# Optimization experiments

Hardware: AMD Instinct MI355X
Metric: run time of the kernel (lower is better)

Reference implementation:

```python
import jax, jax.numpy as jnp
import numpy as np

N, E = 50000, 800000
F_IN, HID, OUT, H = 128, 32, 4, 8
NEG_SLOPE = 0.2


def gat_conv(x, src, dst, W, a_src, a_dst, b):
    """PyG GATConv (concat=True, eval mode). x: [N,Fin]; src/dst: [E'] (self-loops included).
    W: [Fin, Hh*C]; a_src/a_dst: [Hh, C]; b: [Hh*C]."""
    n = x.shape[0]
    Hh, C = a_src.shape
    h = (x @ W).reshape(n, Hh, C)                      # [N,H,C]
    alpha_src = jnp.einsum('nhc,hc->nh', h, a_src)     # [N,H]
    alpha_dst = jnp.einsum('nhc,hc->nh', h, a_dst)     # [N,H]
    alpha = jax.nn.leaky_relu(alpha_src[src] + alpha_dst[dst], NEG_SLOPE)  # [E',H]
    # segment softmax over incoming edges of each dst node
    amax = jax.ops.segment_max(alpha, dst, num_segments=n)  # [N,H]
    ex = jnp.exp(alpha - amax[dst])
    denom = jax.ops.segment_sum(ex, dst, num_segments=n)    # [N,H]
    w = ex / (denom[dst] + 1e-16)                            # [E',H]
    msg = h[src] * w[:, :, None]                             # [E',H,C]
    out = jax.ops.segment_sum(msg, dst, num_segments=n)     # [N,H,C]
    return out.reshape(n, Hh * C) + b


def setup_inputs() -> dict:
    key = jax.random.key(0)
    ks = jax.random.split(key, 9)
    x = jax.random.normal(ks[0], (N, F_IN), jnp.float32)
    # random edge list without self loops (PyG GATConv removes then re-adds self loops)
    rng = np.random.default_rng(0)
    s = rng.integers(0, N, size=E)
    d = rng.integers(0, N, size=E)
    d = np.where(d == s, (d + 1) % N, d)
    edge_index = jnp.asarray(np.stack([s, d]), dtype=jnp.int32)
    g = lambda k, shape, fan: jax.random.normal(k, shape, jnp.float32) * (1.0 / np.sqrt(fan))
    W1 = g(ks[1], (F_IN, H * HID), F_IN)
    a_src1 = g(ks[2], (H, HID), HID)
    a_dst1 = g(ks[3], (H, HID), HID)
    b1 = jnp.zeros((H * HID,), jnp.float32)
    W2 = g(ks[4], (H * HID, H * OUT), H * HID)
    a_src2 = g(ks[5], (H, OUT), OUT)
    a_dst2 = g(ks[6], (H, OUT), OUT)
    b2 = jnp.zeros((H * OUT,), jnp.float32)
    return {"x": x, "edge_index": edge_index, "W1": W1, "a_src1": a_src1,
            "a_dst1": a_dst1, "b1": b1, "W2": W2, "a_src2": a_src2,
            "a_dst2": a_dst2, "b2": b2}


def reference(x, edge_index, W1, a_src1, a_dst1, b1, W2, a_src2, a_dst2, b2):
    n = x.shape[0]
    loops = jnp.arange(n, dtype=edge_index.dtype)
    src = jnp.concatenate([edge_index[0], loops])
    dst = jnp.concatenate([edge_index[1], loops])
    # layer 1 (dropout_edge / dropout are no-ops in eval mode)
    h = gat_conv(x, src, dst, W1, a_src1, a_dst1, b1)
    h = jax.nn.leaky_relu(h, NEG_SLOPE)
    # final layer (concat=True per the original code) -> [N, OUT*H]
    out = gat_conv(h, src, dst, W2, a_src2, a_dst2, b2)
    return out
```

## Files before the change

### kernel.cpp

```cpp
#include <hip/hip_runtime.h>
#include <hip/hip_bf16.h>
#include <cstdint>
#include <cstddef>


__device__ __forceinline__ float lrelu(float a) { return a > 0.f ? a : 0.2f * a; }

__device__ __forceinline__ unsigned short f2bf(float f) {
  unsigned u = __float_as_uint(f);
  unsigned r = (u + 0x7fff + ((u >> 16) & 1)) >> 16;
  return (unsigned short)r;
}
__device__ __forceinline__ float bf_lo(unsigned q) { return __uint_as_float(q << 16); }
__device__ __forceinline__ float bf_hi(unsigned q) { return __uint_as_float(q & 0xffff0000u); }

typedef __attribute__((ext_vector_type(8))) short bf16x8;
typedef __attribute__((ext_vector_type(4))) float f32x4;

#define ROWCAP 64


__global__ __launch_bounds__(256) void k_scatter(const int* __restrict__ srce,
                                                 const int* __restrict__ dste, int E, int n,
                                                 int* __restrict__ cursor,
                                                 int* __restrict__ srcs,
                                                 const float* __restrict__ W1,
                                                 unsigned short* __restrict__ W1T,
                                                 const float* __restrict__ W2,
                                                 unsigned short* __restrict__ W2T) {
  int t = blockIdx.x * 256 + threadIdx.x;
  if (t < E + n) {
    int s, d;
    if (t < E) { s = srce[t]; d = dste[t]; } else { s = d = t - E; }
    int pos = atomicAdd(&cursor[d], 1);
    srcs[(d << 6) + pos] = s;
  }
  if (t < 32768) {
    int k = t >> 8;
    int nn = t & 255;
    W1T[nn * 128 + k] = f2bf(W1[k * 256 + nn]);
  }
  if (t < 8192) {
    int k = t >> 5;
    int nn = t & 31;
    W2T[nn * 256 + k] = f2bf(W2[k * 32 + nn]);
  }
}


__global__ __launch_bounds__(256) void gemm1_mfma(const float* __restrict__ X,
                                                  const unsigned short* __restrict__ WT,
                                                  const float* __restrict__ a_src,
                                                  const float* __restrict__ a_dst,
                                                  unsigned short* __restrict__ h1,
                                                  float* __restrict__ a_s1,
                                                  float* __restrict__ a_d1,
                                                  int M) {
  __shared__ unsigned short As[64 * 136];
  __shared__ unsigned short Bs[256 * 72];
  const int row0 = blockIdx.x * 64;
  const int tid = threadIdx.x;
  const int wv = tid >> 6, lane = tid & 63;
  const int quad = lane >> 4, l15 = lane & 15;
  const int colw = wv * 64;

#pragma unroll
  for (int i = 0; i < 8; i++) {
    int j = tid + 256 * i;
    int r = j >> 5;
    int c4 = (j & 31) * 4;
    float4 v = make_float4(0.f, 0.f, 0.f, 0.f);
    if (row0 + r < M) v = *(const float4*)&X[(size_t)(row0 + r) * 128 + c4];
    uint2 p;
    p.x = (unsigned)f2bf(v.x) | ((unsigned)f2bf(v.y) << 16);
    p.y = (unsigned)f2bf(v.z) | ((unsigned)f2bf(v.w) << 16);
    *(uint2*)&As[r * 136 + c4] = p;
  }

  f32x4 acc[16];
#pragma unroll
  for (int i = 0; i < 16; i++) acc[i] = (f32x4)0.f;

  for (int kc = 0; kc < 128; kc += 64) {
    __syncthreads();
#pragma unroll
    for (int i = 0; i < 8; i++) {
      int j = tid + 256 * i;
      int nn = j >> 3;
      int kg = (j & 7) * 8;
      *(uint4*)&Bs[nn * 72 + kg] = *(const uint4*)&WT[nn * 128 + kc + kg];
    }
    __syncthreads();
#pragma unroll
    for (int ks = 0; ks < 64; ks += 32) {
      bf16x8 af[4], bfr[4];
#pragma unroll
      for (int mi = 0; mi < 4; mi++)
        af[mi] = *(const bf16x8*)&As[(mi * 16 + l15) * 136 + kc + ks + quad * 8];
#pragma unroll
      for (int ni = 0; ni < 4; ni++)
        bfr[ni] = *(const bf16x8*)&Bs[(colw + ni * 16 + l15) * 72 + ks + quad * 8];
#pragma unroll
      for (int mi = 0; mi < 4; mi++)
#pragma unroll
        for (int ni = 0; ni < 4; ni++)
          acc[mi * 4 + ni] = __builtin_amdgcn_mfma_f32_16x16x32_bf16(
              af[mi], bfr[ni], acc[mi * 4 + ni], 0, 0, 0);
    }
  }

  float as_[4], ad_[4];
#pragma unroll
  for (int ni = 0; ni < 4; ni++) {
    int nn = colw + ni * 16 + l15;
    as_[ni] = a_src[nn];
    ad_[ni] = a_dst[nn];
  }
  const int h0 = colw >> 5;
#pragma unroll
  for (int mi = 0; mi < 4; mi++) {
#pragma unroll
    for (int r = 0; r < 4; r++) {
      int m = row0 + mi * 16 + quad * 4 + r;
      bool valid = (m < M);
      if (valid) {
#pragma unroll
        for (int ni = 0; ni < 4; ni++)
          h1[(size_t)m * 256 + colw + ni * 16 + l15] = f2bf(acc[mi * 4 + ni][r]);
      }
      float s0 = fmaf(acc[mi * 4 + 0][r], as_[0], acc[mi * 4 + 1][r] * as_[1]);
      float s1 = fmaf(acc[mi * 4 + 2][r], as_[2], acc[mi * 4 + 3][r] * as_[3]);
      float d0 = fmaf(acc[mi * 4 + 0][r], ad_[0], acc[mi * 4 + 1][r] * ad_[1]);
      float d1 = fmaf(acc[mi * 4 + 2][r], ad_[2], acc[mi * 4 + 3][r] * ad_[3]);
#pragma unroll
      for (int mk = 1; mk <= 8; mk <<= 1) {
        s0 += __shfl_xor(s0, mk);
        s1 += __shfl_xor(s1, mk);
        d0 += __shfl_xor(d0, mk);
        d1 += __shfl_xor(d1, mk);
      }
      if (l15 == 0 && valid) {
        a_s1[m * 8 + h0]     = s0;
        a_s1[m * 8 + h0 + 1] = s1;
        a_d1[m * 8 + h0]     = d0;
        a_d1[m * 8 + h0 + 1] = d1;
      }
    }
  }
}


__global__ __launch_bounds__(256) void gemm2_mfma(const unsigned short* __restrict__ Xb,
                                                  const unsigned short* __restrict__ W2T,
                                                  const float* __restrict__ a_src,
                                                  const float* __restrict__ a_dst,
                                                  unsigned short* __restrict__ h2,
                                                  float* __restrict__ a_s2,
                                                  float* __restrict__ a_d2, int M) {
  __shared__ unsigned short As[64 * 264];
  __shared__ unsigned short Bs[32 * 264];
  const int row0 = blockIdx.x * 64;
  const int tid = threadIdx.x;
  const int wv = tid >> 6, lane = tid & 63;
  const int quad = lane >> 4, l15 = lane & 15;

#pragma unroll
  for (int i = 0; i < 8; i++) {
    int j = tid + 256 * i;
    int r = j >> 5;
    int c8 = (j & 31) * 8;
    uint4 v = make_uint4(0, 0, 0, 0);
    if (row0 + r < M) v = *(const uint4*)&Xb[(size_t)(row0 + r) * 256 + c8];
    *(uint4*)&As[r * 264 + c8] = v;
  }
#pragma unroll
  for (int i = 0; i < 4; i++) {
    int j = tid + 256 * i;
    int nn = j >> 5;
    int kg = (j & 31) * 8;
    *(uint4*)&Bs[nn * 264 + kg] = *(const uint4*)&W2T[nn * 256 + kg];
  }
  __syncthreads();

  f32x4 acc[2];
  acc[0] = (f32x4)0.f;
  acc[1] = (f32x4)0.f;
  const int mr = wv * 16;
#pragma unroll
  for (int ks = 0; ks < 256; ks += 32) {
    bf16x8 af = *(const bf16x8*)&As[(mr + l15) * 264 + ks + quad * 8];
    bf16x8 b0 = *(const bf16x8*)&Bs[(l15) * 264 + ks + quad * 8];
    bf16x8 b1 = *(const bf16x8*)&Bs[(16 + l15) * 264 + ks + quad * 8];
    acc[0] = __builtin_amdgcn_mfma_f32_16x16x32_bf16(af, b0, acc[0], 0, 0, 0);
    acc[1] = __builtin_amdgcn_mfma_f32_16x16x32_bf16(af, b1, acc[1], 0, 0, 0);
  }

  float as_[2], ad_[2];
#pragma unroll
  for (int ni = 0; ni < 2; ni++) {
    int c = ni * 16 + l15;
    as_[ni] = a_src[c];
    ad_[ni] = a_dst[c];
  }
#pragma unroll
  for (int r = 0; r < 4; r++) {
    int m = row0 + mr + quad * 4 + r;
    bool valid = (m < M);
    float s0 = acc[0][r] * as_[0];
    float s1 = acc[1][r] * as_[1];
    float d0 = acc[0][r] * ad_[0];
    float d1 = acc[1][r] * ad_[1];
#pragma unroll
    for (int mk = 1; mk <= 2; mk <<= 1) {
      s0 += __shfl_xor(s0, mk);
      s1 += __shfl_xor(s1, mk);
      d0 += __shfl_xor(d0, mk);
      d1 += __shfl_xor(d1, mk);
    }
    if (valid) {
      h2[(size_t)m * 32 + l15]      = f2bf(acc[0][r]);
      h2[(size_t)m * 32 + 16 + l15] = f2bf(acc[1][r]);
      if ((l15 & 3) == 0) {
        int hq = l15 >> 2;
        a_s2[m * 8 + hq]     = s0;
        a_s2[m * 8 + 4 + hq] = s1;
        a_d2[m * 8 + hq]     = d0;
        a_d2[m * 8 + 4 + hq] = d1;
      }
    }
  }
}


__global__ __launch_bounds__(256) void gat_agg_l1(const unsigned short* __restrict__ h,
                                                  const float* __restrict__ asrc,
                                                  const float* __restrict__ adst,
                                                  const int* __restrict__ rowcnt,
                                                  const int* __restrict__ srcs,
                                                  const float* __restrict__ bias,
                                                  unsigned short* __restrict__ out, int n) {
  int wave = threadIdx.x >> 6;
  int lane = threadIdx.x & 63;
  int d = blockIdx.x * 4 + wave;
  if (d >= n) return;
  int begin = d << 6;
  int end = begin + rowcnt[d];
  int hh = lane & 7;
  float ad = adst[d * 8 + hh];

  const int myhead = lane >> 3;
  float denom = 0.f;
  float4 acc0 = make_float4(0.f, 0.f, 0.f, 0.f);
  float4 acc1 = make_float4(0.f, 0.f, 0.f, 0.f);
#define ACCA(ff, qq)                                        \
    acc0.x = fmaf(ff, bf_lo(qq.x), acc0.x);                 \
    acc0.y = fmaf(ff, bf_hi(qq.x), acc0.y);                 \
    acc0.z = fmaf(ff, bf_lo(qq.y), acc0.z);                 \
    acc0.w = fmaf(ff, bf_hi(qq.y), acc0.w);
#define ACCB(ff, qq)                                        \
    acc1.x = fmaf(ff, bf_lo(qq.x), acc1.x);                 \
    acc1.y = fmaf(ff, bf_hi(qq.x), acc1.y);                 \
    acc1.z = fmaf(ff, bf_lo(qq.y), acc1.z);                 \
    acc1.w = fmaf(ff, bf_hi(qq.y), acc1.w);

  int e = begin;
  for (; e + 16 <= end; e += 16) {
    int s[16];
#pragma unroll
    for (int j = 0; j < 16; j++) s[j] = srcs[e + j];
    float w[16];
    if (lane < 8) {
#pragma unroll
      for (int j = 0; j < 16; j++) {
        w[j] = __expf(lrelu(asrc[s[j] * 8 + lane] + ad));
        denom += w[j];
      }
    } else {
#pragma unroll
      for (int j = 0; j < 16; j++) w[j] = 0.f;
    }
    uint2 q[16];
#pragma unroll
    for (int j = 0; j < 16; j++) q[j] = *(const uint2*)&h[(size_t)s[j] * 256 + lane * 4];
    float f[16];
#pragma unroll
    for (int j = 0; j < 16; j++) f[j] = __shfl(w[j], myhead);
#pragma unroll
    for (int j = 0; j < 16; j += 2) {
      ACCA(f[j], q[j])
      ACCB(f[j + 1], q[j + 1])
    }
  }
  for (; e < end; e += 8) {
    int s[8];
    float w[8];
#pragma unroll
    for (int j = 0; j < 8; j++) {
      int ee = e + j;
      s[j] = srcs[ee < end ? ee : end - 1];
    }
    if (lane < 8) {
#pragma unroll
      for (int j = 0; j < 8; j++) {
        float v = __expf(lrelu(asrc[s[j] * 8 + lane] + ad));
        w[j] = (e + j < end) ? v : 0.f;
        denom += w[j];
      }
    } else {
#pragma unroll
      for (int j = 0; j < 8; j++) w[j] = 0.f;
    }
    uint2 q[8];
#pragma unroll
    for (int j = 0; j < 8; j++) q[j] = *(const uint2*)&h[(size_t)s[j] * 256 + lane * 4];
    float f[8];
#pragma unroll
    for (int j = 0; j < 8; j++) f[j] = __shfl(w[j], myhead);
#pragma unroll
    for (int j = 0; j < 8; j += 2) {
      ACCA(f[j], q[j])
      ACCB(f[j + 1], q[j + 1])
    }
  }
#undef ACCA
#undef ACCB
  float4 acc;
  acc.x = acc0.x + acc1.x;
  acc.y = acc0.y + acc1.y;
  acc.z = acc0.z + acc1.z;
  acc.w = acc0.w + acc1.w;
  float dn = __shfl(denom, myhead) + 1e-16f;
  float inv = 1.f / dn;
  int f = lane * 4;
  float4 bv = *(const float4*)&bias[f];
  float rx = lrelu(acc.x * inv + bv.x);
  float ry = lrelu(acc.y * inv + bv.y);
  float rz = lrelu(acc.z * inv + bv.z);
  float rw = lrelu(acc.w * inv + bv.w);
  uint2 p;
  p.x = (unsigned)f2bf(rx) | ((unsigned)f2bf(ry) << 16);
  p.y = (unsigned)f2bf(rz) | ((unsigned)f2bf(rw) << 16);
  *(uint2*)&out[(size_t)d * 256 + f] = p;
}

__global__ __launch_bounds__(256) void gat_agg_l2(const unsigned short* __restrict__ h,
                                                  const float* __restrict__ asrc,
                                                  const float* __restrict__ adst,
                                                  const int* __restrict__ rowcnt,
                                                  const int* __restrict__ srcs,
                                                  const float* __restrict__ bias,
                                                  float* __restrict__ out, int n) {
  int wave = threadIdx.x >> 6;
  int lane = threadIdx.x & 63;
  int d = blockIdx.x * 4 + wave;
  if (d >= n) return;
  int begin = d << 6;
  int end = begin + rowcnt[d];
  int hh = lane & 7;
  int eg = lane >> 3;
  float ad = adst[d * 8 + hh];

  float denom = 0.f;
  float4 acc = make_float4(0.f, 0.f, 0.f, 0.f);
  for (int base = begin; base < end; base += 32) {
    int eA = base + eg;
    int eB = base + 8 + eg;
    int eC = base + 16 + eg;
    int eD = base + 24 + eg;
    bool vA = eA < end, vB = eB < end, vC = eC < end, vD = eD < end;
    int sA = srcs[vA ? eA : begin];
    int sB = srcs[vB ? eB : begin];
    int sC = srcs[vC ? eC : begin];
    int sD = srcs[vD ? eD : begin];
    float aA = asrc[sA * 8 + hh];
    float aB = asrc[sB * 8 + hh];
    float aC = asrc[sC * 8 + hh];
    float aD = asrc[sD * 8 + hh];
    uint2 qA = *(const uint2*)&h[(size_t)sA * 32 + hh * 4];
    uint2 qB = *(const uint2*)&h[(size_t)sB * 32 + hh * 4];
    uint2 qC = *(const uint2*)&h[(size_t)sC * 32 + hh * 4];
    uint2 qD = *(const uint2*)&h[(size_t)sD * 32 + hh * 4];
    float wA = vA ? __expf(lrelu(aA + ad)) : 0.f;
    float wB = vB ? __expf(lrelu(aB + ad)) : 0.f;
    float wC = vC ? __expf(lrelu(aC + ad)) : 0.f;
    float wD = vD ? __expf(lrelu(aD + ad)) : 0.f;
    denom += (wA + wB) + (wC + wD);
    acc.x = fmaf(wA, bf_lo(qA.x), acc.x); acc.y = fmaf(wA, bf_hi(qA.x), acc.y);
    acc.z = fmaf(wA, bf_lo(qA.y), acc.z); acc.w = fmaf(wA, bf_hi(qA.y), acc.w);
    acc.x = fmaf(wB, bf_lo(qB.x), acc.x); acc.y = fmaf(wB, bf_hi(qB.x), acc.y);
    acc.z = fmaf(wB, bf_lo(qB.y), acc.z); acc.w = fmaf(wB, bf_hi(qB.y), acc.w);
    acc.x = fmaf(wC, bf_lo(qC.x), acc.x); acc.y = fmaf(wC, bf_hi(qC.x), acc.y);
    acc.z = fmaf(wC, bf_lo(qC.y), acc.z); acc.w = fmaf(wC, bf_hi(qC.y), acc.w);
    acc.x = fmaf(wD, bf_lo(qD.x), acc.x); acc.y = fmaf(wD, bf_hi(qD.x), acc.y);
    acc.z = fmaf(wD, bf_lo(qD.y), acc.z); acc.w = fmaf(wD, bf_hi(qD.y), acc.w);
  }
#pragma unroll
  for (int mask = 8; mask <= 32; mask <<= 1) {
    denom += __shfl_xor(denom, mask);
    acc.x += __shfl_xor(acc.x, mask);
    acc.y += __shfl_xor(acc.y, mask);
    acc.z += __shfl_xor(acc.z, mask);
    acc.w += __shfl_xor(acc.w, mask);
  }
  if (lane < 8) {
    float inv = 1.f / (denom + 1e-16f);
    int f = lane * 4;
    float4 bv = *(const float4*)&bias[f];
    float4 r;
    r.x = acc.x * inv + bv.x;
    r.y = acc.y * inv + bv.y;
    r.z = acc.z * inv + bv.z;
    r.w = acc.w * inv + bv.w;
    *(float4*)&out[(size_t)d * 32 + f] = r;
  }
}


extern "C" void kernel_launch(void* const* d_in, const int* in_sizes, int n_in,
                              void* d_out, int out_size, void* d_ws, size_t ws_size,
                              hipStream_t stream) {
  const float* x   = (const float*)d_in[0];
  const int*   ei  = (const int*)d_in[1];
  const float* W1  = (const float*)d_in[2];
  const float* as1 = (const float*)d_in[3];
  const float* ad1 = (const float*)d_in[4];
  const float* b1  = (const float*)d_in[5];
  const float* W2  = (const float*)d_in[6];
  const float* as2 = (const float*)d_in[7];
  const float* ad2 = (const float*)d_in[8];
  const float* b2  = (const float*)d_in[9];
  float* out = (float*)d_out;

  const int E = in_sizes[1] / 2;
  const int n = in_sizes[0] / 128;
  const int* srce = ei;
  const int* dste = ei + E;

  char* ws = (char*)d_ws;
  size_t off = 0;
  auto alloc = [&](size_t bytes) -> void* {
    void* p = ws + off;
    off = (off + bytes + 255) & ~(size_t)255;
    return p;
  };
  int* cursor   = (int*)alloc((size_t)n * 4);
  int* srcs     = (int*)alloc((size_t)n * ROWCAP * 4);
  unsigned short* h1  = (unsigned short*)alloc((size_t)n * 256 * 2);
  unsigned short* w1t = (unsigned short*)alloc((size_t)256 * 128 * 2);
  unsigned short* w2t = (unsigned short*)alloc((size_t)32 * 256 * 2);
  float* a_s1   = (float*)alloc((size_t)n * 8 * 4);
  float* a_d1   = (float*)alloc((size_t)n * 8 * 4);
  unsigned short* x2 = (unsigned short*)alloc((size_t)n * 256 * 2);
  unsigned short* h2 = (unsigned short*)alloc((size_t)n * 32 * 2);
  float* a_s2   = (float*)alloc((size_t)n * 8 * 4);
  float* a_d2   = (float*)alloc((size_t)n * 8 * 4);

  const int tot = E + n;
  hipMemsetAsync(cursor, 0, (size_t)n * 4, stream);
  k_scatter<<<(tot + 255) / 256, 256, 0, stream>>>(srce, dste, E, n, cursor, srcs,
                                                   W1, w1t, W2, w2t);

  gemm1_mfma<<<(n + 63) / 64, 256, 0, stream>>>(x, w1t, as1, ad1, h1, a_s1, a_d1, n);
  gat_agg_l1<<<(n + 3) / 4, 256, 0, stream>>>(h1, a_s1, a_d1, cursor, srcs, b1, x2, n);

  gemm2_mfma<<<(n + 63) / 64, 256, 0, stream>>>(x2, w2t, as2, ad2, h2, a_s2, a_d2, n);
  gat_agg_l2<<<(n + 3) / 4, 256, 0, stream>>>(h2, a_s2, a_d2, cursor, srcs, b2, out, n);
}
```

Measured before the change: 268.4 us.

## Fold attention vectors into weights and compute per-lane softmax weights in aggregation

Precomputes W·a_src and W·a_dst as extra 16-column bf16 weight matrices so both GEMMs produce the attention logits with one additional MFMA, replacing the shuffle-reduction epilogues. In the layer-1 aggregation kernel, every lane now computes its own head's exp weight and denominator instead of 8 lanes computing and broadcasting via shuffles. This trades shuffles and serial dependencies for redundant exp and asrc loads (8x duplicated per head), and rounds the folded attention weights to bf16, which may reduce logit precision.

```diff
diff --git a/kernel.cpp b/kernel.cpp
--- a/kernel.cpp
+++ b/kernel.cpp
@@ -27,7 +27,13 @@
                                                  const float* __restrict__ W1,
                                                  unsigned short* __restrict__ W1T,
                                                  const float* __restrict__ W2,
-                                                 unsigned short* __restrict__ W2T) {
+                                                 unsigned short* __restrict__ W2T,
+                                                 const float* __restrict__ as1,
+                                                 const float* __restrict__ ad1,
+                                                 const float* __restrict__ as2,
+                                                 const float* __restrict__ ad2,
+                                                 unsigned short* __restrict__ Wa1T,
+                                                 unsigned short* __restrict__ Wa2T) {
   int t = blockIdx.x * 256 + threadIdx.x;
   if (t < E + n) {
     int s, d;
@@ -45,19 +51,39 @@
     int nn = t & 31;
     W2T[nn * 256 + k] = f2bf(W2[k * 32 + nn]);
   }
+  if (t < 2048) {
+    int j = t >> 7;
+    int k = t & 127;
+    const float* av = (j < 8) ? &as1[j * 32] : &ad1[(j - 8) * 32];
+    const float* wv = &W1[k * 256 + (j & 7) * 32];
+    float s = 0.f;
+#pragma unroll
+    for (int c = 0; c < 32; c++) s += wv[c] * av[c];
+    Wa1T[j * 128 + k] = f2bf(s);
+  }
+  if (t < 4096) {
+    int j = t >> 8;
+    int k = t & 255;
+    const float* av = (j < 8) ? &as2[j * 4] : &ad2[(j - 8) * 4];
+    const float* wv = &W2[k * 32 + (j & 7) * 4];
+    float s = 0.f;
+#pragma unroll
+    for (int c = 0; c < 4; c++) s += wv[c] * av[c];
+    Wa2T[j * 256 + k] = f2bf(s);
+  }
 }
 
 
 __global__ __launch_bounds__(256) void gemm1_mfma(const float* __restrict__ X,
                                                   const unsigned short* __restrict__ WT,
-                                                  const float* __restrict__ a_src,
-                                                  const float* __restrict__ a_dst,
+                                                  const unsigned short* __restrict__ WaT,
                                                   unsigned short* __restrict__ h1,
                                                   float* __restrict__ a_s1,
                                                   float* __restrict__ a_d1,
                                                   int M) {
   __shared__ unsigned short As[64 * 136];
   __shared__ unsigned short Bs[256 * 72];
+  __shared__ unsigned short Was[16 * 72];
   const int row0 = blockIdx.x * 64;
   const int tid = threadIdx.x;
   const int wv = tid >> 6, lane = tid & 63;
@@ -80,6 +106,7 @@
   f32x4 acc[16];
 #pragma unroll
   for (int i = 0; i < 16; i++) acc[i] = (f32x4)0.f;
+  f32x4 acca = (f32x4)0.f;
 
   for (int kc = 0; kc < 128; kc += 64) {
     __syncthreads();
@@ -90,6 +117,11 @@
       int kg = (j & 7) * 8;
       *(uint4*)&Bs[nn * 72 + kg] = *(const uint4*)&WT[nn * 128 + kc + kg];
     }
+    if (tid < 128) {
+      int j = tid >> 3;
+      int kg = (tid & 7) * 8;
+      *(uint4*)&Was[j * 72 + kg] = *(const uint4*)&WaT[j * 128 + kc + kg];
+    }
     __syncthreads();
 #pragma unroll
     for (int ks = 0; ks < 64; ks += 32) {
@@ -106,45 +138,30 @@
         for (int ni = 0; ni < 4; ni++)
           acc[mi * 4 + ni] = __builtin_amdgcn_mfma_f32_16x16x32_bf16(
               af[mi], bfr[ni], acc[mi * 4 + ni], 0, 0, 0);
-    }
-  }
-
-  float as_[4], ad_[4];
-#pragma unroll
-  for (int ni = 0; ni < 4; ni++) {
-    int nn = colw + ni * 16 + l15;
-    as_[ni] = a_src[nn];
-    ad_[ni] = a_dst[nn];
-  }
-  const int h0 = colw >> 5;
+      bf16x8 afa = *(const bf16x8*)&As[(wv * 16 + l15) * 136 + kc + ks + quad * 8];
+      bf16x8 bfa = *(const bf16x8*)&Was[l15 * 72 + ks + quad * 8];
+      acca = __builtin_amdgcn_mfma_f32_16x16x32_bf16(afa, bfa, acca, 0, 0, 0);
+    }
+  }
+
 #pragma unroll
   for (int mi = 0; mi < 4; mi++) {
 #pragma unroll
     for (int r = 0; r < 4; r++) {
       int m = row0 + mi * 16 + quad * 4 + r;
-      bool valid = (m < M);
-      if (valid) {
+      if (m < M) {
 #pragma unroll
         for (int ni = 0; ni < 4; ni++)
           h1[(size_t)m * 256 + colw + ni * 16 + l15] = f2bf(acc[mi * 4 + ni][r]);
       }
-      float s0 = fmaf(acc[mi * 4 + 0][r], as_[0], acc[mi * 4 + 1][r] * as_[1]);
-      float s1 = fmaf(acc[mi * 4 + 2][r], as_[2], acc[mi * 4 + 3][r] * as_[3]);
-      float d0 = fmaf(acc[mi * 4 + 0][r], ad_[0], acc[mi * 4 + 1][r] * ad_[1]);
-      float d1 = fmaf(acc[mi * 4 + 2][r], ad_[2], acc[mi * 4 + 3][r] * ad_[3]);
-#pragma unroll
-      for (int mk = 1; mk <= 8; mk <<= 1) {
-        s0 += __shfl_xor(s0, mk);
-        s1 += __shfl_xor(s1, mk);
-        d0 += __shfl_xor(d0, mk);
-        d1 += __shfl_xor(d1, mk);
-      }
-      if (l15 == 0 && valid) {
-        a_s1[m * 8 + h0]     = s0;
-        a_s1[m * 8 + h0 + 1] = s1;
-        a_d1[m * 8 + h0]     = d0;
-        a_d1[m * 8 + h0 + 1] = d1;
-      }
+    }
+  }
+#pragma unroll
+  for (int r = 0; r < 4; r++) {
+    int m = row0 + wv * 16 + quad * 4 + r;
+    if (m < M) {
+      if (l15 < 8) a_s1[m * 8 + l15] = acca[r];
+      else         a_d1[m * 8 + (l15 - 8)] = acca[r];
     }
   }
 }
@@ -152,13 +169,13 @@
 
 __global__ __launch_bounds__(256) void gemm2_mfma(const unsigned short* __restrict__ Xb,
                                                   const unsigned short* __restrict__ W2T,
-                                                  const float* __restrict__ a_src,
-                                                  const float* __restrict__ a_dst,
+                                                  const unsigned short* __restrict__ WaT,
                                                   unsigned short* __restrict__ h2,
                                                   float* __restrict__ a_s2,
                                                   float* __restrict__ a_d2, int M) {
   __shared__ unsigned short As[64 * 264];
   __shared__ unsigned short Bs[32 * 264];
+  __shared__ unsigned short Was[16 * 264];
   const int row0 = blockIdx.x * 64;
   const int tid = threadIdx.x;
   const int wv = tid >> 6, lane = tid & 63;
@@ -180,53 +197,39 @@
     int kg = (j & 31) * 8;
     *(uint4*)&Bs[nn * 264 + kg] = *(const uint4*)&W2T[nn * 256 + kg];
   }
+#pragma unroll
+  for (int i = 0; i < 2; i++) {
+    int j = tid + 256 * i;
+    int nn = j >> 5;
+    int kg = (j & 31) * 8;
+    *(uint4*)&Was[nn * 264 + kg] = *(const uint4*)&WaT[nn * 256 + kg];
+  }
   __syncthreads();
 
   f32x4 acc[2];
   acc[0] = (f32x4)0.f;
   acc[1] = (f32x4)0.f;
+  f32x4 acca = (f32x4)0.f;
   const int mr = wv * 16;
 #pragma unroll
   for (int ks = 0; ks < 256; ks += 32) {
     bf16x8 af = *(const bf16x8*)&As[(mr + l15) * 264 + ks + quad * 8];
     bf16x8 b0 = *(const bf16x8*)&Bs[(l15) * 264 + ks + quad * 8];
     bf16x8 b1 = *(const bf16x8*)&Bs[(16 + l15) * 264 + ks + quad * 8];
+    bf16x8 ba = *(const bf16x8*)&Was[(l15) * 264 + ks + quad * 8];
     acc[0] = __builtin_amdgcn_mfma_f32_16x16x32_bf16(af, b0, acc[0], 0, 0, 0);
     acc[1] = __builtin_amdgcn_mfma_f32_16x16x32_bf16(af, b1, acc[1], 0, 0, 0);
-  }
-
-  float as_[2], ad_[2];
-#pragma unroll
-  for (int ni = 0; ni < 2; ni++) {
-    int c = ni * 16 + l15;
-    as_[ni] = a_src[c];
-    ad_[ni] = a_dst[c];
-  }
+    acca   = __builtin_amdgcn_mfma_f32_16x16x32_bf16(af, ba, acca, 0, 0, 0);
+  }
+
 #pragma unroll
   for (int r = 0; r < 4; r++) {
     int m = row0 + mr + quad * 4 + r;
-    bool valid = (m < M);
-    float s0 = acc[0][r] * as_[0];
-    float s1 = acc[1][r] * as_[1];
-    float d0 = acc[0][r] * ad_[0];
-    float d1 = acc[1][r] * ad_[1];
-#pragma unroll
-    for (int mk = 1; mk <= 2; mk <<= 1) {
-      s0 += __shfl_xor(s0, mk);
-      s1 += __shfl_xor(s1, mk);
-      d0 += __shfl_xor(d0, mk);
-      d1 += __shfl_xor(d1, mk);
-    }
-    if (valid) {
+    if (m < M) {
       h2[(size_t)m * 32 + l15]      = f2bf(acc[0][r]);
       h2[(size_t)m * 32 + 16 + l15] = f2bf(acc[1][r]);
-      if ((l15 & 3) == 0) {
-        int hq = l15 >> 2;
-        a_s2[m * 8 + hq]     = s0;
-        a_s2[m * 8 + 4 + hq] = s1;
-        a_d2[m * 8 + hq]     = d0;
-        a_d2[m * 8 + 4 + hq] = d1;
-      }
+      if (l15 < 8) a_s2[m * 8 + l15] = acca[r];
+      else         a_d2[m * 8 + (l15 - 8)] = acca[r];
     }
   }
 }
@@ -245,10 +248,9 @@
   if (d >= n) return;
   int begin = d << 6;
   int end = begin + rowcnt[d];
-  int hh = lane & 7;
-  float ad = adst[d * 8 + hh];
-
   const int myhead = lane >> 3;
+  float ad = adst[d * 8 + myhead];
+
   float denom = 0.f;
   float4 acc0 = make_float4(0.f, 0.f, 0.f, 0.f);
   float4 acc1 = make_float4(0.f, 0.f, 0.f, 0.f);
@@ -268,58 +270,42 @@
     int s[16];
 #pragma unroll
     for (int j = 0; j < 16; j++) s[j] = srcs[e + j];
+    uint2 q[16];
+#pragma unroll
+    for (int j = 0; j < 16; j++) q[j] = *(const uint2*)&h[(size_t)s[j] * 256 + lane * 4];
     float w[16];
-    if (lane < 8) {
-#pragma unroll
-      for (int j = 0; j < 16; j++) {
-        w[j] = __expf(lrelu(asrc[s[j] * 8 + lane] + ad));
-        denom += w[j];
-      }
-    } else {
-#pragma unroll
-      for (int j = 0; j < 16; j++) w[j] = 0.f;
-    }
-    uint2 q[16];
-#pragma unroll
-    for (int j = 0; j < 16; j++) q[j] = *(const uint2*)&h[(size_t)s[j] * 256 + lane * 4];
-    float f[16];
-#pragma unroll
-    for (int j = 0; j < 16; j++) f[j] = __shfl(w[j], myhead);
+#pragma unroll
+    for (int j = 0; j < 16; j++) {
+      w[j] = __expf(lrelu(asrc[s[j] * 8 + myhead] + ad));
+      denom += w[j];
+    }
 #pragma unroll
     for (int j = 0; j < 16; j += 2) {
-      ACCA(f[j], q[j])
-      ACCB(f[j + 1], q[j + 1])
+      ACCA(w[j], q[j])
+      ACCB(w[j + 1], q[j + 1])
     }
   }
   for (; e < end; e += 8) {
     int s[8];
-    float w[8];
 #pragma unroll
     for (int j = 0; j < 8; j++) {
       int ee = e + j;
       s[j] = srcs[ee < end ? ee : end - 1];
     }
-    if (lane < 8) {
-#pragma unroll
-      for (int j = 0; j < 8; j++) {
-        float v = __expf(lrelu(asrc[s[j] * 8 + lane] + ad));
-        w[j] = (e + j < end) ? v : 0.f;
-        denom += w[j];
-      }
-    } else {
-#pragma unroll
-      for (int j = 0; j < 8; j++) w[j] = 0.f;
-    }
     uint2 q[8];
 #pragma unroll
     for (int j = 0; j < 8; j++) q[j] = *(const uint2*)&h[(size_t)s[j] * 256 + lane * 4];
-    float f[8];
-#pragma unroll
-    for (int j = 0; j < 8; j++) f[j] = __shfl(w[j], myhead);
+    float w[8];
+#pragma unroll
+    for (int j = 0; j < 8; j++) {
+      float v = __expf(lrelu(asrc[s[j] * 8 + myhead] + ad));
+      w[j] = (e + j < end) ? v : 0.f;
+      denom += w[j];
+    }
 #pragma unroll
     for (int j = 0; j < 8; j += 2) {
-      ACCA(f[j], q[j])
-      ACCB(f[j + 1], q[j + 1])
+      ACCA(w[j], q[j])
+      ACCB(w[j + 1], q[j + 1])
     }
   }
 #undef ACCA
@@ -329,8 +315,7 @@
   acc.y = acc0.y + acc1.y;
   acc.z = acc0.z + acc1.z;
   acc.w = acc0.w + acc1.w;
-  float dn = __shfl(denom, myhead) + 1e-16f;
-  float inv = 1.f / dn;
+  float inv = 1.f / (denom + 1e-16f);
   int f = lane * 4;
   float4 bv = *(const float4*)&bias[f];
   float rx = lrelu(acc.x * inv + bv.x);
@@ -448,6 +433,8 @@
   unsigned short* h1  = (unsigned short*)alloc((size_t)n * 256 * 2);
   unsigned short* w1t = (unsigned short*)alloc((size_t)256 * 128 * 2);
   unsigned short* w2t = (unsigned short*)alloc((size_t)32 * 256 * 2);
+  unsigned short* wa1t = (unsigned short*)alloc((size_t)16 * 128 * 2);
+  unsigned short* wa2t = (unsigned short*)alloc((size_t)16 * 256 * 2);
   float* a_s1   = (float*)alloc((size_t)n * 8 * 4);
   float* a_d1   = (float*)alloc((size_t)n * 8 * 4);
   unsigned short* x2 = (unsigned short*)alloc((size_t)n * 256 * 2);
@@ -458,11 +445,12 @@
   const int tot = E + n;
   hipMemsetAsync(cursor, 0, (size_t)n * 4, stream);
   k_scatter<<<(tot + 255) / 256, 256, 0, stream>>>(srce, dste, E, n, cursor, srcs,
-                                                   W1, w1t, W2, w2t);
-
-  gemm1_mfma<<<(n + 63) / 64, 256, 0, stream>>>(x, w1t, as1, ad1, h1, a_s1, a_d1, n);
+                                                   W1, w1t, W2, w2t,
+                                                   as1, ad1, as2, ad2, wa1t, wa2t);
+
+  gemm1_mfma<<<(n + 63) / 64, 256, 0, stream>>>(x, w1t, wa1t, h1, a_s1, a_d1, n);
   gat_agg_l1<<<(n + 3) / 4, 256, 0, stream>>>(h1, a_s1, a_d1, cursor, srcs, b1, x2, n);
 
-  gemm2_mfma<<<(n + 63) / 64, 256, 0, stream>>>(x2, w2t, as2, ad2, h2, a_s2, a_d2, n);
+  gemm2_mfma<<<(n + 63) / 64, 256, 0, stream>>>(x2, w2t, wa2t, h2, a_s2, a_d2, n);
   gat_agg_l2<<<(n + 3) / 4, 256, 0, stream>>>(h2, a_s2, a_d2, cursor, srcs, b2, out, n);
 }
```

Result: no change. 269.5 us (+0.4%).
